# Kernel tuning notes

Measured on AMD Instinct MI355X. Metric: run time of the kernel, lower is better.

Reference implementation:

```python
import jax, jax.numpy as jnp
import numpy as np

N, C, G = 50000, 30, 1000   # cells, classes, genes
E = 800000                   # edges
OUT = 8                      # GATv2 out channels, heads=1


def setup_inputs() -> dict:
    key = jax.random.key(0)
    ks = jax.random.split(key, 12)
    X = jax.random.normal(ks[0], (N, G), dtype=jnp.float32)
    Mu = jax.random.normal(ks[1], (C, G), dtype=jnp.float32)
    Var = jax.random.uniform(ks[2], (C, G), dtype=jnp.float32) + 0.5  # strictly positive
    edge_index = jax.random.randint(ks[3], (2, E), 0, N, dtype=jnp.int64)
    # learned params
    W = 0.01 * jax.random.normal(ks[4], (N, C), dtype=jnp.float32)   # torch init zeros; small noise for nontrivial P
    S = jnp.ones((N, 1), dtype=jnp.float32)
    sc = 1.0 / np.sqrt(G)
    Wl = sc * jax.random.normal(ks[5], (OUT, G), dtype=jnp.float32)  # lin_l weight
    bl = jnp.zeros((OUT,), dtype=jnp.float32)
    Wr = sc * jax.random.normal(ks[6], (OUT, G), dtype=jnp.float32)  # lin_r weight
    br = jnp.zeros((OUT,), dtype=jnp.float32)
    att = jax.random.normal(ks[7], (OUT,), dtype=jnp.float32) / np.sqrt(OUT)
    return {"X": X, "Mu": Mu, "Var": Var, "edge_index": edge_index,
            "W": W, "S": S, "Wl": Wl, "bl": bl, "Wr": Wr, "br": br, "att": att}


def reference(X, Mu, Var, edge_index, W, S, Wl, bl, Wr, br, att):
    n = X.shape[0]
    P = jax.nn.softmax(W, axis=1)                       # [N,C]
    # Gaussian log-likelihood term. Expand (X - Mu*S)^2/Var summed over genes:
    invVar = 1.0 / Var                                  # [C,G]
    A = (X * X) @ invVar.T                              # [N,C]  sum X^2/Var
    B = X @ (Mu * invVar).T                             # [N,C]  sum X*Mu/Var
    D = jnp.sum(Mu * Mu * invVar, axis=1)               # [C]    sum Mu^2/Var
    Fmat = -0.5 * (A - 2.0 * S * B + (S * S) * D[None, :])  # [N,C]
    ll_prot = jnp.sum(P * Fmat) / n

    # GATv2 attention (heads=1, add_self_loops=False)
    x_l = X @ Wl.T + bl                                 # [N,8] source transform
    x_r = X @ Wr.T + br                                 # [N,8] target transform
    src, dst = edge_index[0], edge_index[1]
    m = jax.nn.leaky_relu(x_l[src] + x_r[dst], negative_slope=0.2)  # [E,8]
    e = m @ att                                         # [E]
    # edge-softmax grouped by destination node
    emax = jax.ops.segment_max(e, dst, num_segments=n)  # [N]
    e_exp = jnp.exp(e - emax[dst])                      # [E]
    denom = jax.ops.segment_sum(e_exp, dst, num_segments=n)  # [N]
    alpha = e_exp / (denom[dst] + 1e-16)                # [E]

    ce_space = -jnp.sum(P[src] * alpha[:, None] * jnp.log(P[dst] + 1e-8)) / n
    return ll_prot, ce_space, P
```

## Files before the change

kernel.cpp:

```cpp
#include <hip/hip_runtime.h>
#include <hip/hip_bf16.h>
#include <math.h>

#define N_CELLS 50000
#define C_CLS   30
#define G_GENES 1000
#define E_EDGES 800000
#define KPAD    1024
#define NREP    4

typedef __attribute__((ext_vector_type(8))) short bf16x8;
typedef __attribute__((ext_vector_type(4))) float f32x4;

__device__ __forceinline__ unsigned f2bf_u(float f) {
    unsigned u = __float_as_uint(f);
    return (u + 0x7fffu + ((u >> 16) & 1u)) >> 16;
}
__device__ __forceinline__ unsigned pack2(float lo, float hi) {
    union { __hip_bfloat162 h; unsigned u; } cv;
    cv.h = __float22bfloat162_rn(make_float2(lo, hi));
    return cv.u;
}
__device__ __forceinline__ float bf2f(unsigned short u) {
    return __uint_as_float(((unsigned)u) << 16);
}

__device__ __forceinline__ float lrelu02(float v) { return v > 0.f ? v : 0.2f * v; }

__device__ __forceinline__ void lds_barrier() {
    asm volatile("s_waitcnt lgkmcnt(0)" ::: "memory");
    __builtin_amdgcn_s_barrier();
}

__device__ __forceinline__ void pack_pair(const float4& A, const float4& B,
                                          bf16x8* lin, bf16x8* sq) {
    union { unsigned u[4]; bf16x8 v; } ua, u2;
    ua.u[0] = pack2(A.x, A.y); ua.u[1] = pack2(A.z, A.w);
    ua.u[2] = pack2(B.x, B.y); ua.u[3] = pack2(B.z, B.w);
    u2.u[0] = pack2(A.x * A.x, A.y * A.y); u2.u[1] = pack2(A.z * A.z, A.w * A.w);
    u2.u[2] = pack2(B.x * B.x, B.y * B.y); u2.u[3] = pack2(B.z * B.z, B.w * B.w);
    *lin = ua.v; *sq = u2.v;
}

__device__ __forceinline__ float dp4(int4 a, int4 b) {
    const unsigned* ua = (const unsigned*)&a;
    const unsigned* ub = (const unsigned*)&b;
    float s = 0.f;
#pragma unroll
    for (int i = 0; i < 4; i++) {
        float al = __uint_as_float(ua[i] << 16);
        float ah = __uint_as_float(ua[i] & 0xffff0000u);
        float bl = __uint_as_float(ub[i] << 16);
        float bh = __uint_as_float(ub[i] & 0xffff0000u);
        s += al * bl + ah * bh;
    }
    return s;
}

__global__ void prep_kernel(const float* __restrict__ Mu, const float* __restrict__ Var,
                            const float* __restrict__ Wl, const float* __restrict__ Wr,
                            unsigned short* __restrict__ CoefB, float* __restrict__ Dvec,
                            float* __restrict__ dn4, float* __restrict__ out) {
    const int r = blockIdx.x;
    const int t = threadIdx.x;
    __shared__ float red[256];
    float dacc = 0.f;
    for (int g = t; g < KPAD; g += 256) {
        float v = 0.f;
        if (g < G_GENES) {
            if (r < 30) {
                float iv = 1.0f / Var[r * G_GENES + g];
                float mu = Mu[r * G_GENES + g];
                v = iv;
                dacc += mu * mu * iv;
            } else if (r >= 32) {
                int i = r - 32;
                if (i < 30)      v = Mu[i * G_GENES + g] / Var[i * G_GENES + g];
                else if (i < 38) v = Wl[(i - 30) * G_GENES + g];
                else if (i < 46) v = Wr[(i - 38) * G_GENES + g];
            }
        }
        CoefB[r * KPAD + g] = (unsigned short)f2bf_u(v);
    }
    for (int i = blockIdx.x * 256 + t; i < N_CELLS * NREP * 2; i += 80 * 256) dn4[i] = 0.f;
    if (r == 31 && t < 2) out[t] = 0.f;

    if (r < 30) {
        red[t] = dacc;
        __syncthreads();
        for (int s = 128; s > 0; s >>= 1) {
            if (t < s) red[t] += red[t + s];
            __syncthreads();
        }
        if (t == 0) Dvec[r] = red[0];
    }
}

__global__ __launch_bounds__(128, 3) void main_rows_kernel(
    const float* __restrict__ X, const float* __restrict__ W,
    const float* __restrict__ S, const float* __restrict__ bl,
    const float* __restrict__ br, const unsigned short* __restrict__ CoefB,
    const float* __restrict__ Dvec,
    float* __restrict__ out,
    unsigned short* __restrict__ Pb, unsigned short* __restrict__ Lb,
    float* __restrict__ xl, float* __restrict__ xr)
{
    __shared__ __align__(16) unsigned short Ct[2][80 * 72];

    const int t    = threadIdx.x;
    const int w    = t >> 6;
    const int l    = t & 63;
    const int l15  = l & 15;
    const int quad = l >> 4;
    const int k0q  = quad * 8;
    const int wavebase = blockIdx.x * 32 + w * 16;
    const bool valid = (wavebase < N_CELLS);
    const float* __restrict__ xrow = X + (size_t)(wavebase + l15) * G_GENES;

    const int srow = t >> 3;
    const int scol = (t & 7) << 3;
    const unsigned short* __restrict__ cb0 = &CoefB[srow * KPAD + scol];

    f32x4 acc[5];
#pragma unroll
    for (int i = 0; i < 5; i++) acc[i] = (f32x4){0.f, 0.f, 0.f, 0.f};

    {
#pragma unroll
        for (int j = 0; j < 5; j++) {
            int4 p = *(const int4*)(cb0 + 16 * j * KPAD);
            *(int4*)&Ct[0][(srow + 16 * j) * 72 + scol] = p;
        }
    }
    int4 qb[5];
#pragma unroll
    for (int j = 0; j < 5; j++) qb[j] = *(const int4*)(cb0 + 16 * j * KPAD + 64);

    const float4 z4 = make_float4(0.f, 0.f, 0.f, 0.f);
    float4 xs[2][4];
#pragma unroll
    for (int sl = 0; sl < 2; sl++)
#pragma unroll
        for (int i = 0; i < 4; i++) xs[sl][i] = z4;
    if (valid) {
        xs[0][0] = *(const float4*)&xrow[k0q];
        xs[0][1] = *(const float4*)&xrow[k0q + 4];
        xs[0][2] = *(const float4*)&xrow[32 + k0q];
        xs[0][3] = *(const float4*)&xrow[32 + k0q + 4];
        xs[1][0] = *(const float4*)&xrow[64 + k0q];
        xs[1][1] = *(const float4*)&xrow[64 + k0q + 4];
        xs[1][2] = *(const float4*)&xrow[96 + k0q];
        xs[1][3] = *(const float4*)&xrow[96 + k0q + 4];
    }
    lds_barrier();

#pragma unroll
    for (int it = 0; it < 16; ++it) {
        const int sl = it & 1;

        float4 t0 = z4, t1 = z4, t2 = z4, t3 = z4;
        if (it < 14) {
            const int kt2 = (it + 2) * 64;
            if (valid) {
                const int ka = kt2 + k0q;
                t0 = *(const float4*)&xrow[ka];
                t1 = *(const float4*)&xrow[ka + 4];
                int kb = kt2 + 32 + k0q;
                if (kb > 992) kb = 0;
                t2 = *(const float4*)&xrow[kb];
                t3 = *(const float4*)&xrow[kb + 4];
            }
        }
        int4 n0, n1, n2, n3, n4;
        if (it < 14) {
            const int kt2 = (it + 2) * 64;
            n0 = *(const int4*)(cb0 + kt2);
            n1 = *(const int4*)(cb0 + 16 * KPAD + kt2);
            n2 = *(const int4*)(cb0 + 32 * KPAD + kt2);
            n3 = *(const int4*)(cb0 + 48 * KPAD + kt2);
            n4 = *(const int4*)(cb0 + 64 * KPAD + kt2);
        }

        bf16x8 va, v2;
        pack_pair(xs[sl][0], xs[sl][1], &va, &v2);
#pragma unroll
        for (int nt = 0; nt < 5; nt++) {
            bf16x8 b = *(const bf16x8*)&Ct[sl][(nt * 16 + l15) * 72 + k0q];
            acc[nt] = __builtin_amdgcn_mfma_f32_16x16x32_bf16(
                nt < 2 ? v2 : va, b, acc[nt], 0, 0, 0);
        }
        pack_pair(xs[sl][2], xs[sl][3], &va, &v2);
#pragma unroll
        for (int nt = 0; nt < 5; nt++) {
            bf16x8 b = *(const bf16x8*)&Ct[sl][(nt * 16 + l15) * 72 + 32 + k0q];
            acc[nt] = __builtin_amdgcn_mfma_f32_16x16x32_bf16(
                nt < 2 ? v2 : va, b, acc[nt], 0, 0, 0);
        }

        if (it < 15) {
            *(int4*)&Ct[sl ^ 1][ srow       * 72 + scol] = qb[0];
            *(int4*)&Ct[sl ^ 1][(srow + 16) * 72 + scol] = qb[1];
            *(int4*)&Ct[sl ^ 1][(srow + 32) * 72 + scol] = qb[2];
            *(int4*)&Ct[sl ^ 1][(srow + 48) * 72 + scol] = qb[3];
            *(int4*)&Ct[sl ^ 1][(srow + 64) * 72 + scol] = qb[4];
            lds_barrier();
        }
        if (it < 14) {
            xs[sl][0] = t0; xs[sl][1] = t1; xs[sl][2] = t2; xs[sl][3] = t3;
            qb[0] = n0; qb[1] = n1; qb[2] = n2; qb[3] = n3; qb[4] = n4;
        }
    }

    if (!valid) return;

    const int rbase = wavebase + quad * 4;
    const bool c2ok = (l15 < 14);
    const float d0 = Dvec[l15];
    const float d1 = c2ok ? Dvec[16 + l15] : 0.f;
    float llacc = 0.f;
#pragma unroll
    for (int r = 0; r < 4; r++) {
        const int row = rbase + r;
        float w0 = W[(size_t)row * 30 + l15];
        float w1 = c2ok ? W[(size_t)row * 30 + 16 + l15] : -1e30f;
        float m = fmaxf(w0, w1);
#pragma unroll
        for (int mm = 1; mm < 16; mm <<= 1) m = fmaxf(m, __shfl_xor(m, mm, 64));
        float e0 = __expf(w0 - m);
        float e1 = c2ok ? __expf(w1 - m) : 0.f;
        float s = e0 + e1;
#pragma unroll
        for (int mm = 1; mm < 16; mm <<= 1) s += __shfl_xor(s, mm, 64);
        float inv = 1.0f / s;
        float p0 = e0 * inv, p1 = e1 * inv;
        float Sn = S[row], Sn2 = Sn * Sn;
        float F0 = -0.5f * (acc[0][r] - 2.0f * Sn * acc[2][r] + Sn2 * d0);
        float F1 = -0.5f * (acc[1][r] - 2.0f * Sn * acc[3][r] + Sn2 * d1);
        float lp = p0 * F0 + (c2ok ? p1 * F1 : 0.f);
#pragma unroll
        for (int mm = 1; mm < 16; mm <<= 1) lp += __shfl_xor(lp, mm, 64);
        llacc += lp;

        out[2 + (size_t)row * 30 + l15] = p0;
        float lg0 = __logf(p0 + 1e-8f);
        Pb[(size_t)row * 32 + l15] = (unsigned short)f2bf_u(p0);
        Lb[(size_t)row * 32 + l15] = (unsigned short)f2bf_u(lg0);
        if (c2ok) {
            out[2 + (size_t)row * 30 + 16 + l15] = p1;
            float lg1 = __logf(p1 + 1e-8f);
            Pb[(size_t)row * 32 + 16 + l15] = (unsigned short)f2bf_u(p1);
            Lb[(size_t)row * 32 + 16 + l15] = (unsigned short)f2bf_u(lg1);
        } else {
            Pb[(size_t)row * 32 + 16 + l15] = 0;
            Lb[(size_t)row * 32 + 16 + l15] = 0;
        }
        if (l15 >= 14)                xl[(size_t)row * 8 + (l15 - 14)] = acc[3][r] + bl[l15 - 14];
        else if (l15 < 6)             xl[(size_t)row * 8 + (l15 + 2)]  = acc[4][r] + bl[l15 + 2];
        if (l15 >= 6 && l15 < 14)     xr[(size_t)row * 8 + (l15 - 6)]  = acc[4][r] + br[l15 - 6];
    }
    llacc += __shfl_xor(llacc, 16, 64);
    llacc += __shfl_xor(llacc, 32, 64);
    if (l == 0) atomicAdd(&out[0], llacc * (1.0f / N_CELLS));
}

__global__ __launch_bounds__(256) void edge_pass(
    const int* __restrict__ ei, const float* __restrict__ xl,
    const float* __restrict__ xr, const float* __restrict__ att,
    const unsigned short* __restrict__ Pb, const unsigned short* __restrict__ Lb,
    float* __restrict__ dn4) {
    const int t = threadIdx.x;
    const int g = t >> 2;
    const int j = t & 3;
    const int e = blockIdx.x * 64 + g;
    const int src = ei[e];
    const int dst = ei[E_EDGES + e];

    float2 lv = *(const float2*)&xl[(size_t)src * 8 + j * 2];
    float2 rv = *(const float2*)&xr[(size_t)dst * 8 + j * 2];
    float2 av = *(const float2*)&att[j * 2];
    float ev = lrelu02(lv.x + rv.x) * av.x + lrelu02(lv.y + rv.y) * av.y;
    ev += __shfl_xor(ev, 1, 64);
    ev += __shfl_xor(ev, 2, 64);
    float p = __expf(ev);

    int4 a = *(const int4*)&Pb[(size_t)src * 32 + j * 8];
    int4 b = *(const int4*)&Lb[(size_t)dst * 32 + j * 8];
    float dot = dp4(a, b);
    dot += __shfl_xor(dot, 1, 64);
    dot += __shfl_xor(dot, 2, 64);

    float* base = &dn4[((size_t)(blockIdx.x & (NREP - 1)) * N_CELLS + dst) * 2];
    if (j == 0)      atomicAdd(base, p);
    else if (j == 1) atomicAdd(base + 1, p * dot);
}

__global__ __launch_bounds__(256) void finalize_kernel(const float* __restrict__ dn4,
                                                       float* __restrict__ out) {
    const int t = threadIdx.x;
    const int i = blockIdx.x * 256 + t;
    float c = 0.f;
    if (i < N_CELLS) {
        float d  = (dn4[(size_t)i * 2]     + dn4[((size_t)N_CELLS + i) * 2]) +
                   (dn4[((size_t)2 * N_CELLS + i) * 2] + dn4[((size_t)3 * N_CELLS + i) * 2]);
        float nm = (dn4[(size_t)i * 2 + 1] + dn4[((size_t)N_CELLS + i) * 2 + 1]) +
                   (dn4[((size_t)2 * N_CELLS + i) * 2 + 1] + dn4[((size_t)3 * N_CELLS + i) * 2 + 1]);
        c = nm / (d + 1e-16f);
    }
#pragma unroll
    for (int m = 1; m < 64; m <<= 1) c += __shfl_xor(c, m, 64);
    __shared__ float wsum[4];
    if ((t & 63) == 0) wsum[t >> 6] = c;
    __syncthreads();
    if (t == 0)
        atomicAdd(&out[1], -(wsum[0] + wsum[1] + wsum[2] + wsum[3]) * (1.0f / N_CELLS));
}

extern "C" void kernel_launch(void* const* d_in, const int* in_sizes, int n_in,
                              void* d_out, int out_size, void* d_ws, size_t ws_size,
                              hipStream_t stream) {
    const float* X   = (const float*)d_in[0];
    const float* Mu  = (const float*)d_in[1];
    const float* Var = (const float*)d_in[2];
    const int*   ei  = (const int*)d_in[3];
    const float* W   = (const float*)d_in[4];
    const float* S   = (const float*)d_in[5];
    const float* Wl  = (const float*)d_in[6];
    const float* bl  = (const float*)d_in[7];
    const float* Wr  = (const float*)d_in[8];
    const float* br  = (const float*)d_in[9];
    const float* att = (const float*)d_in[10];

    float* out = (float*)d_out;

    float* wsf = (float*)d_ws;
    unsigned short* CoefB  = (unsigned short*)wsf;
    float* Dvec            = wsf + 40960;
    unsigned short* Pb     = (unsigned short*)(wsf + 40992);
    unsigned short* Lb     = (unsigned short*)(wsf + 840992);
    float* xl              = wsf + 1640992;
    float* xr              = wsf + 2040992;
    float* dn4             = wsf + 2440992;

    prep_kernel<<<80, 256, 0, stream>>>(Mu, Var, Wl, Wr, CoefB, Dvec, dn4, out);
    main_rows_kernel<<<(N_CELLS + 31) / 32, 128, 0, stream>>>(
        X, W, S, bl, br, CoefB, Dvec, out, Pb, Lb, xl, xr);
    edge_pass<<<E_EDGES / 64, 256, 0, stream>>>(ei, xl, xr, att, Pb, Lb, dn4);
    finalize_kernel<<<(N_CELLS + 255) / 256, 256, 0, stream>>>(dn4, out);
}
```

Baseline: 437.2 us.

## Split K across four waves per 16-row tile with pre-swizzled coefficient layout

```diff
diff --git a/kernel.cpp b/kernel.cpp
--- a/kernel.cpp
+++ b/kernel.cpp
@@ -26,11 +26,6 @@
 }
 
 __device__ __forceinline__ float lrelu02(float v) { return v > 0.f ? v : 0.2f * v; }
-
-__device__ __forceinline__ void lds_barrier() {
-    asm volatile("s_waitcnt lgkmcnt(0)" ::: "memory");
-    __builtin_amdgcn_s_barrier();
-}
 
 __device__ __forceinline__ void pack_pair(const float4& A, const float4& B,
                                           bf16x8* lin, bf16x8* sq) {
@@ -59,28 +54,37 @@
 
 __global__ void prep_kernel(const float* __restrict__ Mu, const float* __restrict__ Var,
                             const float* __restrict__ Wl, const float* __restrict__ Wr,
-                            unsigned short* __restrict__ CoefB, float* __restrict__ Dvec,
+                            unsigned short* __restrict__ CoefT, float* __restrict__ Dvec,
                             float* __restrict__ dn4, float* __restrict__ out) {
     const int r = blockIdx.x;
     const int t = threadIdx.x;
     __shared__ float red[256];
     float dacc = 0.f;
-    for (int g = t; g < KPAD; g += 256) {
-        float v = 0.f;
-        if (g < G_GENES) {
-            if (r < 30) {
-                float iv = 1.0f / Var[r * G_GENES + g];
-                float mu = Mu[r * G_GENES + g];
-                v = iv;
-                dacc += mu * mu * iv;
-            } else if (r >= 32) {
-                int i = r - 32;
-                if (i < 30)      v = Mu[i * G_GENES + g] / Var[i * G_GENES + g];
-                else if (i < 38) v = Wl[(i - 30) * G_GENES + g];
-                else if (i < 46) v = Wr[(i - 38) * G_GENES + g];
+    if (r < 80) {
+        const int nt  = r >> 4;
+        const int l15 = r & 15;
+        for (int g = t; g < KPAD; g += 256) {
+            float v = 0.f;
+            if (g < G_GENES) {
+                if (r < 30) {
+                    float iv = 1.0f / Var[r * G_GENES + g];
+                    float mu = Mu[r * G_GENES + g];
+                    v = iv;
+                    dacc += mu * mu * iv;
+                } else if (r >= 32) {
+                    int i = r - 32;
+                    if (i < 30)      v = Mu[i * G_GENES + g] / Var[i * G_GENES + g];
+                    else if (i < 38) v = Wl[(i - 30) * G_GENES + g];
+                    else if (i < 46) v = Wr[(i - 38) * G_GENES + g];
+                }
             }
+            const int kt = g >> 6;
+            const int ks = (g >> 5) & 1;
+            const int hi = (g & 31) >> 3;
+            const int j  = g & 7;
+            const int l  = hi * 16 + l15;
+            CoefT[((kt * 5 + nt) * 2 + ks) * 512 + l * 8 + j] = (unsigned short)f2bf_u(v);
         }
-        CoefB[r * KPAD + g] = (unsigned short)f2bf_u(v);
     }
     for (int i = blockIdx.x * 256 + t; i < N_CELLS * NREP * 2; i += 80 * 256) dn4[i] = 0.f;
     if (r == 31 && t < 2) out[t] = 0.f;
@@ -96,16 +100,16 @@
     }
 }
 
-__global__ __launch_bounds__(128, 3) void main_rows_kernel(
+__global__ __launch_bounds__(256, 5) void main_rows_kernel(
     const float* __restrict__ X, const float* __restrict__ W,
     const float* __restrict__ S, const float* __restrict__ bl,
-    const float* __restrict__ br, const unsigned short* __restrict__ CoefB,
+    const float* __restrict__ br, const unsigned short* __restrict__ CoefT,
     const float* __restrict__ Dvec,
     float* __restrict__ out,
     unsigned short* __restrict__ Pb, unsigned short* __restrict__ Lb,
     float* __restrict__ xl, float* __restrict__ xr)
 {
-    __shared__ __align__(16) unsigned short Ct[2][80 * 72];
+    __shared__ __align__(16) float cmb[3][64][21];
 
     const int t    = threadIdx.x;
     const int w    = t >> 6;
@@ -113,107 +117,68 @@
     const int l15  = l & 15;
     const int quad = l >> 4;
     const int k0q  = quad * 8;
-    const int wavebase = blockIdx.x * 32 + w * 16;
-    const bool valid = (wavebase < N_CELLS);
-    const float* __restrict__ xrow = X + (size_t)(wavebase + l15) * G_GENES;
-
-    const int srow = t >> 3;
-    const int scol = (t & 7) << 3;
-    const unsigned short* __restrict__ cb0 = &CoefB[srow * KPAD + scol];
+    const int rowbase = blockIdx.x * 16;
+    const float* __restrict__ xrow = X + (size_t)(rowbase + l15) * G_GENES;
+    const unsigned short* __restrict__ ctw = CoefT + (size_t)(w * 4 * 5 * 2) * 512 + l * 8;
 
     f32x4 acc[5];
 #pragma unroll
     for (int i = 0; i < 5; i++) acc[i] = (f32x4){0.f, 0.f, 0.f, 0.f};
 
-    {
-#pragma unroll
-        for (int j = 0; j < 5; j++) {
-            int4 p = *(const int4*)(cb0 + 16 * j * KPAD);
-            *(int4*)&Ct[0][(srow + 16 * j) * 72 + scol] = p;
-        }
-    }
-    int4 qb[5];
-#pragma unroll
-    for (int j = 0; j < 5; j++) qb[j] = *(const int4*)(cb0 + 16 * j * KPAD + 64);
-
-    const float4 z4 = make_float4(0.f, 0.f, 0.f, 0.f);
-    float4 xs[2][4];
-#pragma unroll
-    for (int sl = 0; sl < 2; sl++)
-#pragma unroll
-        for (int i = 0; i < 4; i++) xs[sl][i] = z4;
-    if (valid) {
-        xs[0][0] = *(const float4*)&xrow[k0q];
-        xs[0][1] = *(const float4*)&xrow[k0q + 4];
-        xs[0][2] = *(const float4*)&xrow[32 + k0q];
-        xs[0][3] = *(const float4*)&xrow[32 + k0q + 4];
-        xs[1][0] = *(const float4*)&xrow[64 + k0q];
-        xs[1][1] = *(const float4*)&xrow[64 + k0q + 4];
-        xs[1][2] = *(const float4*)&xrow[96 + k0q];
-        xs[1][3] = *(const float4*)&xrow[96 + k0q + 4];
-    }
-    lds_barrier();
-
-#pragma unroll
-    for (int it = 0; it < 16; ++it) {
-        const int sl = it & 1;
-
-        float4 t0 = z4, t1 = z4, t2 = z4, t3 = z4;
-        if (it < 14) {
-            const int kt2 = (it + 2) * 64;
-            if (valid) {
-                const int ka = kt2 + k0q;
-                t0 = *(const float4*)&xrow[ka];
-                t1 = *(const float4*)&xrow[ka + 4];
-                int kb = kt2 + 32 + k0q;
-                if (kb > 992) kb = 0;
-                t2 = *(const float4*)&xrow[kb];
-                t3 = *(const float4*)&xrow[kb + 4];
-            }
-        }
-        int4 n0, n1, n2, n3, n4;
-        if (it < 14) {
-            const int kt2 = (it + 2) * 64;
-            n0 = *(const int4*)(cb0 + kt2);
-            n1 = *(const int4*)(cb0 + 16 * KPAD + kt2);
-            n2 = *(const int4*)(cb0 + 32 * KPAD + kt2);
-            n3 = *(const int4*)(cb0 + 48 * KPAD + kt2);
-            n4 = *(const int4*)(cb0 + 64 * KPAD + kt2);
-        }
-
+#pragma unroll
+    for (int it = 0; it < 4; ++it) {
+        const int kt   = w * 4 + it;
+        const int kcol = kt * 64;
+
+        float4 a0 = *(const float4*)&xrow[kcol + k0q];
+        float4 a1 = *(const float4*)&xrow[kcol + k0q + 4];
+        int kb = kcol + 32 + k0q;
+        if (kb > 992) kb = 0;
+        float4 a2 = *(const float4*)&xrow[kb];
+        float4 a3 = *(const float4*)&xrow[kb + 4];
+
+        bf16x8 b0 = *(const bf16x8*)&ctw[((it * 5 + 0) * 2 + 0) * 512];
+        bf16x8 b1 = *(const bf16x8*)&ctw[((it * 5 + 1) * 2 + 0) * 512];
+        bf16x8 b2 = *(const bf16x8*)&ctw[((it * 5 + 2) * 2 + 0) * 512];
+        bf16x8 b3 = *(const bf16x8*)&ctw[((it * 5 + 3) * 2 + 0) * 512];
+        bf16x8 b4 = *(const bf16x8*)&ctw[((it * 5 + 4) * 2 + 0) * 512];
         bf16x8 va, v2;
-        pack_pair(xs[sl][0], xs[sl][1], &va, &v2);
-#pragma unroll
-        for (int nt = 0; nt < 5; nt++) {
-            bf16x8 b = *(const bf16x8*)&Ct[sl][(nt * 16 + l15) * 72 + k0q];
-            acc[nt] = __builtin_amdgcn_mfma_f32_16x16x32_bf16(
-                nt < 2 ? v2 : va, b, acc[nt], 0, 0, 0);
-        }
-        pack_pair(xs[sl][2], xs[sl][3], &va, &v2);
-#pragma unroll
-        for (int nt = 0; nt < 5; nt++) {
-            bf16x8 b = *(const bf16x8*)&Ct[sl][(nt * 16 + l15) * 72 + 32 + k0q];
-            acc[nt] = __builtin_amdgcn_mfma_f32_16x16x32_bf16(
-                nt < 2 ? v2 : va, b, acc[nt], 0, 0, 0);
-        }
-
-        if (it < 15) {
-            *(int4*)&Ct[sl ^ 1][ srow       * 72 + scol] = qb[0];
-            *(int4*)&Ct[sl ^ 1][(srow + 16) * 72 + scol] = qb[1];
-            *(int4*)&Ct[sl ^ 1][(srow + 32) * 72 + scol] = qb[2];
-            *(int4*)&Ct[sl ^ 1][(srow + 48) * 72 + scol] = qb[3];
-            *(int4*)&Ct[sl ^ 1][(srow + 64) * 72 + scol] = qb[4];
-            lds_barrier();
-        }
-        if (it < 14) {
-            xs[sl][0] = t0; xs[sl][1] = t1; xs[sl][2] = t2; xs[sl][3] = t3;
-            qb[0] = n0; qb[1] = n1; qb[2] = n2; qb[3] = n3; qb[4] = n4;
-        }
-    }
-
-    if (!valid) return;
-
-    const int rbase = wavebase + quad * 4;
+        pack_pair(a0, a1, &va, &v2);
+        acc[0] = __builtin_amdgcn_mfma_f32_16x16x32_bf16(v2, b0, acc[0], 0, 0, 0);
+        acc[1] = __builtin_amdgcn_mfma_f32_16x16x32_bf16(v2, b1, acc[1], 0, 0, 0);
+        acc[2] = __builtin_amdgcn_mfma_f32_16x16x32_bf16(va, b2, acc[2], 0, 0, 0);
+        acc[3] = __builtin_amdgcn_mfma_f32_16x16x32_bf16(va, b3, acc[3], 0, 0, 0);
+        acc[4] = __builtin_amdgcn_mfma_f32_16x16x32_bf16(va, b4, acc[4], 0, 0, 0);
+
+        b0 = *(const bf16x8*)&ctw[((it * 5 + 0) * 2 + 1) * 512];
+        b1 = *(const bf16x8*)&ctw[((it * 5 + 1) * 2 + 1) * 512];
+        b2 = *(const bf16x8*)&ctw[((it * 5 + 2) * 2 + 1) * 512];
+        b3 = *(const bf16x8*)&ctw[((it * 5 + 3) * 2 + 1) * 512];
+        b4 = *(const bf16x8*)&ctw[((it * 5 + 4) * 2 + 1) * 512];
+        pack_pair(a2, a3, &va, &v2);
+        acc[0] = __builtin_amdgcn_mfma_f32_16x16x32_bf16(v2, b0, acc[0], 0, 0, 0);
+        acc[1] = __builtin_amdgcn_mfma_f32_16x16x32_bf16(v2, b1, acc[1], 0, 0, 0);
+        acc[2] = __builtin_amdgcn_mfma_f32_16x16x32_bf16(va, b2, acc[2], 0, 0, 0);
+        acc[3] = __builtin_amdgcn_mfma_f32_16x16x32_bf16(va, b3, acc[3], 0, 0, 0);
+        acc[4] = __builtin_amdgcn_mfma_f32_16x16x32_bf16(va, b4, acc[4], 0, 0, 0);
+    }
+
+    if (w > 0) {
+#pragma unroll
+        for (int i = 0; i < 5; i++)
+#pragma unroll
+            for (int r = 0; r < 4; r++) cmb[w - 1][l][i * 4 + r] = acc[i][r];
+    }
+    __syncthreads();
+    if (w != 0) return;
+#pragma unroll
+    for (int j = 0; j < 3; j++)
+#pragma unroll
+        for (int i = 0; i < 5; i++)
+#pragma unroll
+            for (int r = 0; r < 4; r++) acc[i][r] += cmb[j][l][i * 4 + r];
+
+    const int rbase = rowbase + quad * 4;
     const bool c2ok = (l15 < 14);
     const float d0 = Dvec[l15];
     const float d1 = c2ok ? Dvec[16 + l15] : 0.f;
@@ -333,7 +298,7 @@
     float* out = (float*)d_out;
 
     float* wsf = (float*)d_ws;
-    unsigned short* CoefB  = (unsigned short*)wsf;
+    unsigned short* CoefT  = (unsigned short*)wsf;
     float* Dvec            = wsf + 40960;
     unsigned short* Pb     = (unsigned short*)(wsf + 40992);
     unsigned short* Lb     = (unsigned short*)(wsf + 840992);
@@ -341,9 +306,9 @@
     float* xr              = wsf + 2040992;
     float* dn4             = wsf + 2440992;
 
-    prep_kernel<<<80, 256, 0, stream>>>(Mu, Var, Wl, Wr, CoefB, Dvec, dn4, out);
-    main_rows_kernel<<<(N_CELLS + 31) / 32, 128, 0, stream>>>(
-        X, W, S, bl, br, CoefB, Dvec, out, Pb, Lb, xl, xr);
+    prep_kernel<<<80, 256, 0, stream>>>(Mu, Var, Wl, Wr, CoefT, Dvec, dn4, out);
+    main_rows_kernel<<<N_CELLS / 16, 256, 0, stream>>>(
+        X, W, S, bl, br, CoefT, Dvec, out, Pb, Lb, xl, xr);
     edge_pass<<<E_EDGES / 64, 256, 0, stream>>>(ei, xl, xr, att, Pb, Lb, dn4);
     finalize_kernel<<<(N_CELLS + 255) / 256, 256, 0, stream>>>(dn4, out);
 }
```

After: 447.4 us. 1.02x slower.
